# Performance work log

Hardware: AMD Instinct MI355X
Metric: run time of the kernel (lower is better)

The kernel has to match this reference:

```python
import jax, jax.numpy as jnp
import numpy as np

B, T, D, H, HD = 2, 2048, 1024, 16, 64
EPS = 1.1920929e-07  # torch.finfo(float32).eps used by F.rms_norm default
VE_GATE_SCALE = 2.0
KEY_OFFSET = True


def rms_norm(x):
    return x * jax.lax.rsqrt(jnp.mean(x * x, axis=-1, keepdims=True) + EPS)


def apply_rotary(x, cos, sin):
    # x: [B,T,H,HD], cos/sin: [T, HD//2]
    c = cos[None, :, None, :]
    s = sin[None, :, None, :]
    x1, x2 = jnp.split(x, 2, axis=-1)
    return jnp.concatenate([x1 * c + x2 * s, -x1 * s + x2 * c], axis=-1)


def setup_inputs() -> dict:
    key = jax.random.key(0)
    ks = jax.random.split(key, 8)
    bound = (3.0 ** 0.5) * (D ** -0.5)
    x = jax.random.normal(ks[0], (B, T, D), dtype=jnp.float32)
    ve = jax.random.normal(ks[1], (B, T, H * HD), dtype=jnp.float32)
    sa_lambdas = jnp.ones((2,), dtype=jnp.float32)
    # realistic RoPE tables
    inv_freq = (10000.0 ** (-np.arange(HD // 2) / (HD // 2))).astype(np.float32)
    ang = np.arange(T, dtype=np.float32)[:, None] * inv_freq[None, :]
    cos = jnp.asarray(np.cos(ang))
    sin = jnp.asarray(np.sin(ang))
    # qkvo weight: uniform init everywhere (orig zeros o-proj; randomized for a non-trivial baseline)
    qkvo_w = jax.random.uniform(ks[2], (4 * D, D), dtype=jnp.float32, minval=-bound, maxval=bound)
    attn_gate_w = 0.02 * jax.random.normal(ks[3], (H, D), dtype=jnp.float32)
    ve_gate_w = 0.02 * jax.random.normal(ks[4], (H, D), dtype=jnp.float32)
    attn_scale = jnp.float32(0.12)
    docs = jnp.sort(jax.random.randint(ks[5], (T,), 0, 8).astype(jnp.int32))
    return {"x": x, "ve": ve, "sa_lambdas": sa_lambdas, "cos": cos, "sin": sin,
            "qkvo_w": qkvo_w, "attn_gate_w": attn_gate_w, "ve_gate_w": ve_gate_w,
            "attn_scale": attn_scale, "docs": docs}


def reference(x, ve, sa_lambdas, cos, sin, qkvo_w, attn_gate_w, ve_gate_w, attn_scale, docs):
    # QKV projection: rows [0:3D] of qkvo_w
    qkv = jnp.einsum('btd,ed->bte', x, sa_lambdas[0] * qkvo_w[:3 * D])
    qkv = qkv.reshape(B, T, 3 * H, HD)
    q, k, v = qkv[:, :, :H], qkv[:, :, H:2 * H], qkv[:, :, 2 * H:]
    q, k = rms_norm(q), rms_norm(k)
    q, k = apply_rotary(q, cos, sin), apply_rotary(k, cos, sin)
    if KEY_OFFSET:
        # shift two head-dim bands of k forward by one position
        k = k.at[:, 1:, :, HD // 4:HD // 2].set(k[:, :-1, :, HD // 4:HD // 2])
        k = k.at[:, 1:, :, 3 * HD // 4:].set(k[:, :-1, :, 3 * HD // 4:])
    # gated value embedding
    ve_gate = VE_GATE_SCALE * jax.nn.sigmoid(jnp.einsum('btd,hd->bth', x, ve_gate_w))
    v = v + ve_gate[..., None] * ve.reshape(B, T, H, HD)
    # causal + document masked attention (score_mod semantics)
    idx = jnp.arange(T)
    mask = (idx[:, None] >= idx[None, :]) & (docs[:, None] == docs[None, :])  # [T,T]
    scores = jnp.einsum('bqhd,bkhd->bhqk', q, k) * attn_scale
    scores = jnp.where(mask[None, None], scores, -jnp.inf)
    p = jax.nn.softmax(scores, axis=-1)
    y = jnp.einsum('bhqk,bkhd->bqhd', p, v)
    # attention output gate
    attn_gate = jax.nn.sigmoid(jnp.einsum('btd,hd->bth', x, attn_gate_w))
    y = y * attn_gate[..., None]
    # output projection: rows [3D:4D]
    y = y.reshape(B, T, H * HD)
    out = jnp.einsum('btd,ed->bte', y, sa_lambdas[1] * qkvo_w[3 * D:])
    return out
```

## Files before the change

kernel.cpp:

```cpp
#include <hip/hip_runtime.h>
#include <math.h>

#define B_ 2
#define T_ 2048
#define D_ 1024
#define H_ 16
#define HD_ 64
#define EPS_ 1.1920929e-07f
#define VE_SCALE_ 2.0f
#define QN_ 3200

typedef __bf16 bf16_t;
typedef __bf16 bf16x4 __attribute__((ext_vector_type(4)));
typedef __bf16 bf16x8 __attribute__((ext_vector_type(8)));
typedef float f32x4 __attribute__((ext_vector_type(4)));

__device__ const f32x4 F4ZERO = {0.f, 0.f, 0.f, 0.f};

typedef __attribute__((address_space(1))) const void gvoid_t;
typedef __attribute__((address_space(3))) void lvoid_t;

__device__ __forceinline__ void gl_lds16(const bf16_t* g, bf16_t* l) {
  __builtin_amdgcn_global_load_lds((gvoid_t*)g, (lvoid_t*)l, 16, 0, 0);
}

__global__ __launch_bounds__(256) void cast_bf16(
    const float* __restrict__ in, bf16_t* __restrict__ out, int n4)
{
  const int i = blockIdx.x * 256 + threadIdx.x;
  if (i >= n4) return;
  const float4 v = ((const float4*)in)[i];
  bf16x4 o = {(bf16_t)v.x, (bf16_t)v.y, (bf16_t)v.z, (bf16_t)v.w};
  ((bf16x4*)out)[i] = o;
}

__global__ __launch_bounds__(256) void gemm_bf16(
    const bf16_t* __restrict__ A, const bf16_t* __restrict__ W,
    void* __restrict__ Cout, int M, int N, int K,
    const float* __restrict__ lam, int li, int n_scaled, int out_bf)
{
  const float scale = lam[li];
  __shared__ bf16_t As[128][64];
  __shared__ bf16_t Bs[128][64];
  const int tid = threadIdx.x;
  const int lane = tid & 63, w = tid >> 6;
  const int lr = lane & 15, lg = lane >> 4;
  const int wr = w >> 1, wc = w & 1;

  const int nwg = gridDim.x * gridDim.y;
  int bid = blockIdx.y * gridDim.x + blockIdx.x;
  bid = (bid & 7) * (nwg >> 3) + (bid >> 3);
  const int row0 = (bid / gridDim.x) * 128;
  const int col0 = (bid % gridDim.x) * 128;

  const int rl = lane >> 3;
  const int cg = (lane & 7) ^ rl;
  const bf16_t* Ag = A + (size_t)(row0 + w * 32 + rl) * K + cg * 8;
  const bf16_t* Wg = W + (size_t)(col0 + w * 32 + rl) * K + cg * 8;
  bf16_t* AsW = &As[w * 32][0];
  bf16_t* BsW = &Bs[w * 32][0];

  f32x4 acc[4][4];
#pragma unroll
  for (int i = 0; i < 4; ++i)
#pragma unroll
    for (int j = 0; j < 4; ++j) acc[i][j] = F4ZERO;

  const int sA = lr & 7;
  const int c0 = (lg ^ sA) * 8;
  const int c1 = c0 ^ 32;

  for (int k0 = 0; k0 < K; k0 += 64) {
    __syncthreads();
#pragma unroll
    for (int i = 0; i < 4; ++i) {
      gl_lds16(Ag + (size_t)(i * 8) * K + k0, AsW + i * 512);
      gl_lds16(Wg + (size_t)(i * 8) * K + k0, BsW + i * 512);
    }
    __syncthreads();

    bf16x8 af[4], bfr[4];
#pragma unroll
    for (int fm = 0; fm < 4; ++fm)
      af[fm] = *(const bf16x8*)&As[wr * 64 + fm * 16 + lr][c0];
#pragma unroll
    for (int fn = 0; fn < 4; ++fn)
      bfr[fn] = *(const bf16x8*)&Bs[wc * 64 + fn * 16 + lr][c0];
#pragma unroll
    for (int fm = 0; fm < 4; ++fm)
#pragma unroll
      for (int fn = 0; fn < 4; ++fn)
        acc[fm][fn] = __builtin_amdgcn_mfma_f32_16x16x32_bf16(
            af[fm], bfr[fn], acc[fm][fn], 0, 0, 0);
#pragma unroll
    for (int fm = 0; fm < 4; ++fm)
      af[fm] = *(const bf16x8*)&As[wr * 64 + fm * 16 + lr][c1];
#pragma unroll
    for (int fn = 0; fn < 4; ++fn)
      bfr[fn] = *(const bf16x8*)&Bs[wc * 64 + fn * 16 + lr][c1];
#pragma unroll
    for (int fm = 0; fm < 4; ++fm)
#pragma unroll
      for (int fn = 0; fn < 4; ++fn)
        acc[fm][fn] = __builtin_amdgcn_mfma_f32_16x16x32_bf16(
            af[fm], bfr[fn], acc[fm][fn], 0, 0, 0);
  }
#pragma unroll
  for (int fm = 0; fm < 4; ++fm)
#pragma unroll
    for (int fn = 0; fn < 4; ++fn)
#pragma unroll
      for (int r = 0; r < 4; ++r) {
        const int row = row0 + wr * 64 + fm * 16 + lg * 4 + r;
        const int col = col0 + wc * 64 + fn * 16 + lr;
        const float v = acc[fm][fn][r] * ((col < n_scaled) ? scale : 1.f);
        if (out_bf) ((bf16_t*)Cout)[(size_t)row * N + col] = (bf16_t)v;
        else        ((float*)Cout)[(size_t)row * N + col] = v;
      }
}

__global__ __launch_bounds__(256) void post_kernel(
    const bf16_t* __restrict__ qkv_b, const float* __restrict__ ve,
    const float* __restrict__ cosb, const float* __restrict__ sinb,
    bf16_t* __restrict__ q_bf, bf16_t* __restrict__ k_bf,
    bf16_t* __restrict__ v_bf, float* __restrict__ attn_gate)
{
  const int wid = (blockIdx.x * blockDim.x + threadIdx.x) >> 6;
  const int lane = threadIdx.x & 63;
  const int h = wid & (H_ - 1);
  const int t = (wid >> 4) & (T_ - 1);
  const int b = wid >> 15;
  const size_t row = (size_t)(b * T_ + t) * QN_;
  const float qraw = (float)qkv_b[row + h * HD_ + lane];
  const float kraw = (float)qkv_b[row + D_ + h * HD_ + lane];
  const float vraw = (float)qkv_b[row + 2 * D_ + h * HD_ + lane];
  const float c = cosb[t * (HD_ / 2) + (lane & 31)];
  const float s = sinb[t * (HD_ / 2) + (lane & 31)];

  float ssq = qraw * qraw;
  float ssk = kraw * kraw;
#pragma unroll
  for (int off = 32; off > 0; off >>= 1) {
    ssq += __shfl_xor(ssq, off);
    ssk += __shfl_xor(ssk, off);
  }
  const float qn = qraw * rsqrtf(ssq * (1.f / 64.f) + EPS_);
  const float kn = kraw * rsqrtf(ssk * (1.f / 64.f) + EPS_);
  const float qpartner = __shfl_xor(qn, 32);
  const float kpartner = __shfl_xor(kn, 32);
  const float qo = (lane < 32) ? fmaf(qn, c, qpartner * s)
                               : fmaf(qn, c, -qpartner * s);
  const float ko = (lane < 32) ? fmaf(kn, c, kpartner * s)
                               : fmaf(kn, c, -kpartner * s);
  const int bh = b * H_ + h;
  const size_t oidx = ((size_t)bh * T_ + t) * HD_ + lane;
  q_bf[oidx] = (bf16_t)qo;
  k_bf[oidx] = (bf16_t)ko;
  const float gv = VE_SCALE_ / (1.f + __expf(-(float)qkv_b[row + 3088 + h]));
  const float vv = fmaf(gv, ve[(size_t)(b * T_ + t) * D_ + h * HD_ + lane], vraw);
  v_bf[oidx] = (bf16_t)vv;
  if (lane == 0)
    attn_gate[(b * T_ + t) * H_ + h] =
        1.f / (1.f + __expf(-(float)qkv_b[row + 3072 + h]));
}

__global__ __launch_bounds__(256) void attn_mfma(
    const bf16_t* __restrict__ q_buf, const bf16_t* __restrict__ k_tmp,
    const bf16_t* __restrict__ v_buf, const float* __restrict__ attn_gate,
    const int* __restrict__ docs, const float* __restrict__ scale_ptr,
    bf16_t* __restrict__ y_buf)
{
  const int qt = blockIdx.x, bh = blockIdx.y;
  const int b = bh >> 4, h = bh & 15;
  const int tid = threadIdx.x;
  const int w = tid >> 6, lane = tid & 63;
  const int lr = lane & 15, lg = lane >> 4;
  const float scale = scale_ptr[0];
  __shared__ bf16_t Ks[64][72];
  __shared__ bf16_t Vt[64][72];
  __shared__ bf16_t Ps[64][72];
  __shared__ int dk[64];

  const int dlo = docs[qt * 64];
  const unsigned long long bal =
      __ballot((lane <= qt) && (docs[lane * 64 + 63] >= dlo));
  const int ktlo = __ffsll(bal) - 1;

  const bf16_t* qp = q_buf + ((size_t)bh * T_ + qt * 64 + w * 16 + lr) * HD_;
  const bf16x8 aq0 = *(const bf16x8*)(qp + lg * 8);
  const bf16x8 aq1 = *(const bf16x8*)(qp + 32 + lg * 8);
  int qpos_r[4], docq_r[4];
#pragma unroll
  for (int r = 0; r < 4; ++r) {
    qpos_r[r] = qt * 64 + w * 16 + lg * 4 + r;
    docq_r[r] = docs[qpos_r[r]];
  }
  f32x4 acc[4];
#pragma unroll
  for (int fn = 0; fn < 4; ++fn) acc[fn] = F4ZERO;
  float m[4] = {-1e30f, -1e30f, -1e30f, -1e30f};
  float l[4] = {0.f, 0.f, 0.f, 0.f};

#pragma unroll 1
  for (int kt = ktlo; kt <= qt; ++kt) {
    __syncthreads();
#pragma unroll
    for (int i = 0; i < 2; ++i) {
      const int idx = i * 256 + tid;
      const int krow = idx >> 3;
      const int c8 = (idx & 7) << 3;
      const int gk = kt * 64 + krow;
      const int gks = (((c8 & 16) != 0) && gk > 0) ? gk - 1 : gk;
      *(bf16x8*)&Ks[krow][c8] =
          *(const bf16x8*)(k_tmp + ((size_t)bh * T_ + gks) * HD_ + c8);
      const int kpos = idx & 63;
      const int d0 = (idx >> 6) << 3;
      const bf16x8 vv =
          *(const bf16x8*)(v_buf + ((size_t)bh * T_ + kt * 64 + kpos) * HD_ + d0);
#pragma unroll
      for (int j = 0; j < 8; ++j) Vt[d0 + j][kpos] = vv[j];
    }
    if (tid < 64) dk[tid] = docs[kt * 64 + tid];
    __syncthreads();

    f32x4 s[4];
#pragma unroll
    for (int fn = 0; fn < 4; ++fn) {
      const bf16x8 bk0 = *(const bf16x8*)&Ks[fn * 16 + lr][lg * 8];
      const bf16x8 bk1 = *(const bf16x8*)&Ks[fn * 16 + lr][32 + lg * 8];
      f32x4 z = F4ZERO;
      z = __builtin_amdgcn_mfma_f32_16x16x32_bf16(aq0, bk0, z, 0, 0, 0);
      s[fn] = __builtin_amdgcn_mfma_f32_16x16x32_bf16(aq1, bk1, z, 0, 0, 0);
    }
    const bool strict = (kt < qt);
#pragma unroll
    for (int fn = 0; fn < 4; ++fn) {
      const int kd = dk[fn * 16 + lr];
      const int kp = kt * 64 + fn * 16 + lr;
#pragma unroll
      for (int r = 0; r < 4; ++r) {
        const bool valid = (kd == docq_r[r]) && (strict || kp <= qpos_r[r]);
        s[fn][r] = valid ? s[fn][r] * scale : -3.0e38f;
      }
    }
#pragma unroll
    for (int r = 0; r < 4; ++r) {
      float cm = fmaxf(fmaxf(s[0][r], s[1][r]), fmaxf(s[2][r], s[3][r]));
      cm = fmaxf(cm, __shfl_xor(cm, 1));
      cm = fmaxf(cm, __shfl_xor(cm, 2));
      cm = fmaxf(cm, __shfl_xor(cm, 4));
      cm = fmaxf(cm, __shfl_xor(cm, 8));
      const float mn = fmaxf(m[r], cm);
      const float sc = __expf(m[r] - mn);
      m[r] = mn;
      const float p0 = __expf(s[0][r] - mn);
      const float p1 = __expf(s[1][r] - mn);
      const float p2 = __expf(s[2][r] - mn);
      const float p3 = __expf(s[3][r] - mn);
      float ps = (p0 + p1) + (p2 + p3);
      ps += __shfl_xor(ps, 1);
      ps += __shfl_xor(ps, 2);
      ps += __shfl_xor(ps, 4);
      ps += __shfl_xor(ps, 8);
      l[r] = l[r] * sc + ps;
      acc[0][r] *= sc; acc[1][r] *= sc; acc[2][r] *= sc; acc[3][r] *= sc;
      const int prow = w * 16 + lg * 4 + r;
      Ps[prow][0 + lr]  = (bf16_t)p0;
      Ps[prow][16 + lr] = (bf16_t)p1;
      Ps[prow][32 + lr] = (bf16_t)p2;
      Ps[prow][48 + lr] = (bf16_t)p3;
    }
    const bf16x8 ap0 = *(const bf16x8*)&Ps[w * 16 + lr][lg * 8];
    const bf16x8 ap1 = *(const bf16x8*)&Ps[w * 16 + lr][32 + lg * 8];
#pragma unroll
    for (int fn = 0; fn < 4; ++fn) {
      const bf16x8 bv0 = *(const bf16x8*)&Vt[fn * 16 + lr][lg * 8];
      const bf16x8 bv1 = *(const bf16x8*)&Vt[fn * 16 + lr][32 + lg * 8];
      acc[fn] = __builtin_amdgcn_mfma_f32_16x16x32_bf16(ap0, bv0, acc[fn], 0, 0, 0);
      acc[fn] = __builtin_amdgcn_mfma_f32_16x16x32_bf16(ap1, bv1, acc[fn], 0, 0, 0);
    }
  }
#pragma unroll
  for (int r = 0; r < 4; ++r) {
    const float inv = attn_gate[(size_t)(b * T_ + qpos_r[r]) * H_ + h] / l[r];
#pragma unroll
    for (int fn = 0; fn < 4; ++fn)
      y_buf[(size_t)(b * T_ + qpos_r[r]) * D_ + h * HD_ + fn * 16 + lr] =
          (bf16_t)(acc[fn][r] * inv);
  }
}

extern "C" void kernel_launch(void* const* d_in, const int* in_sizes, int n_in,
                              void* d_out, int out_size, void* d_ws, size_t ws_size,
                              hipStream_t stream) {
  const float* x    = (const float*)d_in[0];
  const float* ve   = (const float*)d_in[1];
  const float* lam  = (const float*)d_in[2];
  const float* cosb = (const float*)d_in[3];
  const float* sinb = (const float*)d_in[4];
  const float* qkvo = (const float*)d_in[5];
  const float* agw  = (const float*)d_in[6];
  const float* vgw  = (const float*)d_in[7];
  const float* ascl = (const float*)d_in[8];
  const int*   docs = (const int*)d_in[9];
  float* out = (float*)d_out;

  const size_t BT = (size_t)B_ * T_;
  float* cur = (float*)d_ws;
  bf16_t* x_bf = (bf16_t*)cur;        cur += BT * D_ / 2;
  bf16_t* wq_bf = (bf16_t*)cur;       cur += (size_t)QN_ * D_ / 2;
  bf16_t* wo_bf = (bf16_t*)cur;       cur += (size_t)D_ * D_ / 2;
  bf16_t* qkv_b = (bf16_t*)cur;       cur += BT * QN_ / 2;
  bf16_t* q_bf = (bf16_t*)cur;        cur += BT * D_ / 2;
  bf16_t* k_bf = (bf16_t*)cur;        cur += BT * D_ / 2;
  bf16_t* v_bf = (bf16_t*)cur;        cur += BT * D_ / 2;
  bf16_t* y_bf = (bf16_t*)cur;        cur += BT * D_ / 2;
  float* attn_gate = cur;             cur += BT * H_;

  const int nx4 = (int)(BT * D_ / 4);
  cast_bf16<<<(nx4 + 255) / 256, 256, 0, stream>>>(x, x_bf, nx4);
  const int nwq4 = (int)((size_t)3 * D_ * D_ / 4);
  cast_bf16<<<(nwq4 + 255) / 256, 256, 0, stream>>>(qkvo, wq_bf, nwq4);
  const int ng4 = (int)((size_t)H_ * D_ / 4);
  cast_bf16<<<(ng4 + 255) / 256, 256, 0, stream>>>(agw, wq_bf + (size_t)3072 * D_, ng4);
  cast_bf16<<<(ng4 + 255) / 256, 256, 0, stream>>>(vgw, wq_bf + (size_t)3088 * D_, ng4);
  const int nwo4 = (int)((size_t)D_ * D_ / 4);
  cast_bf16<<<(nwo4 + 255) / 256, 256, 0, stream>>>(qkvo + (size_t)3 * D_ * D_, wo_bf, nwo4);

  gemm_bf16<<<dim3(QN_ / 128, BT / 128), 256, 0, stream>>>(
      x_bf, wq_bf, qkv_b, (int)BT, QN_, D_, lam, 0, 3072, 1);

  post_kernel<<<(B_ * T_ * H_) / 4, 256, 0, stream>>>(
      qkv_b, ve, cosb, sinb, q_bf, k_bf, v_bf, attn_gate);

  attn_mfma<<<dim3(T_ / 64, B_ * H_), 256, 0, stream>>>(
      q_bf, k_bf, v_bf, attn_gate, docs, ascl, y_bf);

  gemm_bf16<<<dim3(D_ / 128, BT / 128), 256, 0, stream>>>(
      y_bf, wo_bf, out, (int)BT, D_, D_, lam, 1, D_, 0);
}
```

Measured before the change: 142.1 us.

## Shrink GEMM K-tile to 32, add MFMA priority hints, merge weight casts

The GEMM K-step drops from 64 to 32. The XOR LDS swizzle and the workgroup-ID remapping are removed, and each warp now issues four global-to-LDS loads per step instead of eight. The attention kernel wraps its MFMA sections with s_setprio to favour matrix issue, and the QKV and O weight casts merge into one launch. The risks are more LDS bank conflicts, twice as many barrier pairs per K, and poorer L2 locality without the block remap.

Measured after the change: 161.0 us. 13.4% more time.

```diff
diff --git a/kernel.cpp b/kernel.cpp
--- a/kernel.cpp
+++ b/kernel.cpp
@@ -34,31 +34,40 @@
   ((bf16x4*)out)[i] = o;
 }
 
+__global__ __launch_bounds__(256) void cast_qkvo(
+    const float* __restrict__ in, bf16_t* __restrict__ wq,
+    bf16_t* __restrict__ wo, int n4, int nsplit4)
+{
+  const int i = blockIdx.x * 256 + threadIdx.x;
+  if (i >= n4) return;
+  const float4 v = ((const float4*)in)[i];
+  bf16x4 o = {(bf16_t)v.x, (bf16_t)v.y, (bf16_t)v.z, (bf16_t)v.w};
+  if (i < nsplit4) ((bf16x4*)wq)[i] = o;
+  else             ((bf16x4*)wo)[i - nsplit4] = o;
+}
+
 __global__ __launch_bounds__(256) void gemm_bf16(
     const bf16_t* __restrict__ A, const bf16_t* __restrict__ W,
     void* __restrict__ Cout, int M, int N, int K,
     const float* __restrict__ lam, int li, int n_scaled, int out_bf)
 {
   const float scale = lam[li];
-  __shared__ bf16_t As[128][64];
-  __shared__ bf16_t Bs[128][64];
+  __shared__ bf16_t As[128][32];
+  __shared__ bf16_t Bs[128][32];
   const int tid = threadIdx.x;
   const int lane = tid & 63, w = tid >> 6;
   const int lr = lane & 15, lg = lane >> 4;
   const int wr = w >> 1, wc = w & 1;
-
-  const int nwg = gridDim.x * gridDim.y;
-  int bid = blockIdx.y * gridDim.x + blockIdx.x;
-  bid = (bid & 7) * (nwg >> 3) + (bid >> 3);
-  const int row0 = (bid / gridDim.x) * 128;
-  const int col0 = (bid % gridDim.x) * 128;
-
-  const int rl = lane >> 3;
-  const int cg = (lane & 7) ^ rl;
-  const bf16_t* Ag = A + (size_t)(row0 + w * 32 + rl) * K + cg * 8;
-  const bf16_t* Wg = W + (size_t)(col0 + w * 32 + rl) * K + cg * 8;
-  bf16_t* AsW = &As[w * 32][0];
-  bf16_t* BsW = &Bs[w * 32][0];
+  const int row0 = blockIdx.y * 128, col0 = blockIdx.x * 128;
+  const int srow = w * 32 + (lane >> 2);
+  const int scol = (lane & 3) * 8;
+  const bf16_t* Ag = A + (size_t)(row0 + srow) * K + scol;
+  const bf16_t* Wg = W + (size_t)(col0 + srow) * K + scol;
+  bf16_t* AsB0 = &As[w * 32][0];
+  bf16_t* AsB1 = &As[w * 32 + 16][0];
+  bf16_t* BsB0 = &Bs[w * 32][0];
+  bf16_t* BsB1 = &Bs[w * 32 + 16][0];
+  const size_t r16 = (size_t)16 * K;
 
   f32x4 acc[4][4];
 #pragma unroll
@@ -66,38 +75,21 @@
 #pragma unroll
     for (int j = 0; j < 4; ++j) acc[i][j] = F4ZERO;
 
-  const int sA = lr & 7;
-  const int c0 = (lg ^ sA) * 8;
-  const int c1 = c0 ^ 32;
-
-  for (int k0 = 0; k0 < K; k0 += 64) {
+  for (int k0 = 0; k0 < K; k0 += 32) {
     __syncthreads();
-#pragma unroll
-    for (int i = 0; i < 4; ++i) {
-      gl_lds16(Ag + (size_t)(i * 8) * K + k0, AsW + i * 512);
-      gl_lds16(Wg + (size_t)(i * 8) * K + k0, BsW + i * 512);
-    }
+    gl_lds16(Ag + k0, AsB0);
+    gl_lds16(Ag + r16 + k0, AsB1);
+    gl_lds16(Wg + k0, BsB0);
+    gl_lds16(Wg + r16 + k0, BsB1);
     __syncthreads();
 
     bf16x8 af[4], bfr[4];
 #pragma unroll
     for (int fm = 0; fm < 4; ++fm)
-      af[fm] = *(const bf16x8*)&As[wr * 64 + fm * 16 + lr][c0];
+      af[fm] = *(const bf16x8*)&As[wr * 64 + fm * 16 + lr][lg * 8];
 #pragma unroll
     for (int fn = 0; fn < 4; ++fn)
-      bfr[fn] = *(const bf16x8*)&Bs[wc * 64 + fn * 16 + lr][c0];
-#pragma unroll
-    for (int fm = 0; fm < 4; ++fm)
-#pragma unroll
-      for (int fn = 0; fn < 4; ++fn)
-        acc[fm][fn] = __builtin_amdgcn_mfma_f32_16x16x32_bf16(
-            af[fm], bfr[fn], acc[fm][fn], 0, 0, 0);
-#pragma unroll
-    for (int fm = 0; fm < 4; ++fm)
-      af[fm] = *(const bf16x8*)&As[wr * 64 + fm * 16 + lr][c1];
-#pragma unroll
-    for (int fn = 0; fn < 4; ++fn)
-      bfr[fn] = *(const bf16x8*)&Bs[wc * 64 + fn * 16 + lr][c1];
+      bfr[fn] = *(const bf16x8*)&Bs[wc * 64 + fn * 16 + lr][lg * 8];
 #pragma unroll
     for (int fm = 0; fm < 4; ++fm)
 #pragma unroll
@@ -224,6 +216,7 @@
     __syncthreads();
 
     f32x4 s[4];
+    __builtin_amdgcn_s_setprio(1);
 #pragma unroll
     for (int fn = 0; fn < 4; ++fn) {
       const bf16x8 bk0 = *(const bf16x8*)&Ks[fn * 16 + lr][lg * 8];
@@ -232,6 +225,7 @@
       z = __builtin_amdgcn_mfma_f32_16x16x32_bf16(aq0, bk0, z, 0, 0, 0);
       s[fn] = __builtin_amdgcn_mfma_f32_16x16x32_bf16(aq1, bk1, z, 0, 0, 0);
     }
+    __builtin_amdgcn_s_setprio(0);
     const bool strict = (kt < qt);
 #pragma unroll
     for (int fn = 0; fn < 4; ++fn) {
@@ -272,6 +266,7 @@
     }
     const bf16x8 ap0 = *(const bf16x8*)&Ps[w * 16 + lr][lg * 8];
     const bf16x8 ap1 = *(const bf16x8*)&Ps[w * 16 + lr][32 + lg * 8];
+    __builtin_amdgcn_s_setprio(1);
 #pragma unroll
     for (int fn = 0; fn < 4; ++fn) {
       const bf16x8 bv0 = *(const bf16x8*)&Vt[fn * 16 + lr][lg * 8];
@@ -279,6 +274,7 @@
       acc[fn] = __builtin_amdgcn_mfma_f32_16x16x32_bf16(ap0, bv0, acc[fn], 0, 0, 0);
       acc[fn] = __builtin_amdgcn_mfma_f32_16x16x32_bf16(ap1, bv1, acc[fn], 0, 0, 0);
     }
+    __builtin_amdgcn_s_setprio(0);
   }
 #pragma unroll
   for (int r = 0; r < 4; ++r) {
@@ -319,13 +315,12 @@
 
   const int nx4 = (int)(BT * D_ / 4);
   cast_bf16<<<(nx4 + 255) / 256, 256, 0, stream>>>(x, x_bf, nx4);
-  const int nwq4 = (int)((size_t)3 * D_ * D_ / 4);
-  cast_bf16<<<(nwq4 + 255) / 256, 256, 0, stream>>>(qkvo, wq_bf, nwq4);
+  const int nq4 = (int)((size_t)4 * D_ * D_ / 4);
+  const int ns4 = (int)((size_t)3 * D_ * D_ / 4);
+  cast_qkvo<<<(nq4 + 255) / 256, 256, 0, stream>>>(qkvo, wq_bf, wo_bf, nq4, ns4);
   const int ng4 = (int)((size_t)H_ * D_ / 4);
-  cast_bf16<<<(ng4 + 255) / 256, 256, 0, stream>>>(agw, wq_bf + (size_t)3072 * D_, ng4);
+  cast_bf16<<<(2 * ng4 + 255) / 256, 256, 0, stream>>>(agw, wq_bf + (size_t)3072 * D_, ng4);
   cast_bf16<<<(ng4 + 255) / 256, 256, 0, stream>>>(vgw, wq_bf + (size_t)3088 * D_, ng4);
-  const int nwo4 = (int)((size_t)D_ * D_ / 4);
-  cast_bf16<<<(nwo4 + 255) / 256, 256, 0, stream>>>(qkvo + (size_t)3 * D_ * D_, wo_bf, nwo4);
 
   gemm_bf16<<<dim3(QN_ / 128, BT / 128), 256, 0, stream>>>(
       x_bf, wq_bf, qkv_b, (int)BT, QN_, D_, lam, 0, 3072, 1);
```
